# Optimization experiments

Measured on AMD Instinct MI355X. Metric: run time of the kernel, lower is better.

Reference implementation:

```python
import jax, jax.numpy as jnp
import numpy as np
from jax import lax

CAP = 15.0
EPS = 1e-6

def _rmsnorm(x, w):
    xf = x.astype(jnp.float32)
    var = jnp.mean(xf * xf, axis=-1, keepdims=True)
    return w * (xf * lax.rsqrt(var + EPS)).astype(x.dtype)

def _softcap_sigmoid(x):
    return jax.nn.sigmoid(CAP * jnp.tanh(x / CAP))

def setup_inputs() -> dict:
    key = jax.random.key(0)
    ks = jax.random.split(key, 4)
    B, S, D, P = 8, 2048, 1024, 1365
    x = jax.random.normal(ks[0], (B, S, D), dtype=jnp.float32)
    h0 = jnp.zeros((B, P), dtype=jnp.float32)
    ln_weight = jnp.ones((D,), dtype=jnp.float32)
    gate_w = jax.random.normal(ks[1], (3 * P, D), dtype=jnp.float32) * 0.02
    cell_w = jax.random.normal(ks[2], (P, D), dtype=jnp.float32) * 0.02
    out_w = jax.random.normal(ks[3], (D, P), dtype=jnp.float32) * 0.02
    return {"x": x, "h0": h0, "ln_weight": ln_weight, "gate_w": gate_w,
            "cell_w": cell_w, "out_w": out_w}

def reference(x, h0, ln_weight, gate_w, cell_w, out_w):
    B, S, D = x.shape
    P = cell_w.shape[0]
    residual = x
    xn = _rmsnorm(x, ln_weight)
    # gates: [B,S,3P] -> [B,S,3,P]
    gates = jnp.einsum('bsd,gd->bsg', xn, gate_w).reshape(B, S, 3, P)
    g = _softcap_sigmoid(gates)
    i_gate, f_gate, o_gate = g[:, :, 0], g[:, :, 1], g[:, :, 2]
    c_input = jnp.einsum('bsd,pd->bsp', xn, cell_w)
    # sequential sLSTM recurrence over time via scan; xs are time-major [S,B,P]
    xs = (jnp.swapaxes(c_input, 0, 1), jnp.swapaxes(i_gate, 0, 1),
          jnp.swapaxes(f_gate, 0, 1), jnp.swapaxes(o_gate, 0, 1))
    def step(h, ts):
        c_t, i_t, f_t, o_t = ts
        h = f_t * h + i_t * jnp.tanh(c_t)
        return h, o_t * jnp.tanh(h)
    h_final, ys = lax.scan(step, h0, xs)
    output = jnp.swapaxes(ys, 0, 1)  # [B,S,P]
    out = residual + jnp.einsum('bsp,dp->bsd', output, out_w)
    return (out, h_final)
```

## Files before the change

### kernel.cpp

```cpp
#include <hip/hip_runtime.h>
#include <hip/hip_bf16.h>
#include <cstdint>

#define B_   8
#define S_   2048
#define D_   1024
#define P_   1365
#define M_   (B_*S_)
#define KP   1408
#define NGCP (4*KP)
#define CHUNK 32
#define CMAX (S_/CHUNK)

typedef __attribute__((ext_vector_type(8))) short bf16x8;
typedef __attribute__((ext_vector_type(4))) float f32x4;

__device__ __forceinline__ float fast_rcp(float x) {
  return __builtin_amdgcn_rcpf(x);
}
__device__ __forceinline__ float fast_tanh(float x) {
  float e = __expf(2.0f * x);
  return 1.0f - 2.0f * fast_rcp(e + 1.0f);
}
__device__ __forceinline__ float softcap_sig(float x) {
  float u = x * (1.0f / 15.0f);
  float z = -x + x * u * u * (1.0f / 3.0f);
  return fast_rcp(1.0f + __expf(z));
}
__device__ __forceinline__ float bf2f(unsigned short u) {
  union { float f; unsigned int i; } x; x.i = ((unsigned)u) << 16; return x.f;
}
__device__ __forceinline__ unsigned short f2bf(float f) {
  __hip_bfloat16 h = __float2bfloat16(f);
  return *reinterpret_cast<unsigned short*>(&h);
}
__device__ __forceinline__ void gload_lds16(const void* g, void* l) {
  __builtin_amdgcn_global_load_lds(
      (const __attribute__((address_space(1))) uint32_t*)g,
      (__attribute__((address_space(3))) uint32_t*)l,
      16, 0, 0);
}

__global__ void k_prep_wgc(const float* __restrict__ gate_w,
                           const float* __restrict__ cell_w,
                           __hip_bfloat16* __restrict__ wgc) {
  int gid = blockIdx.x * blockDim.x + threadIdx.x;
  int idx = gid * 4;
  int r = idx >> 10, c = idx & 1023;
  int g = r / KP;
  int rr = r - g * KP;
  float4 v;
  if (rr < P_) {
    if (g < 3) v = *(const float4*)(gate_w + (size_t)(g * P_ + rr) * D_ + c);
    else       v = *(const float4*)(cell_w + (size_t)rr * D_ + c);
  } else v = make_float4(0.f, 0.f, 0.f, 0.f);
  __hip_bfloat16* dst = wgc + idx;
  dst[0] = __float2bfloat16(v.x); dst[1] = __float2bfloat16(v.y);
  dst[2] = __float2bfloat16(v.z); dst[3] = __float2bfloat16(v.w);
}

__global__ void k_prep_wout(const float* __restrict__ out_w,
                            __hip_bfloat16* __restrict__ wout) {
  int gid = blockIdx.x * blockDim.x + threadIdx.x;
  int idx = gid * 4;
  int d = idx / KP, p = idx - d * KP;
  __hip_bfloat16* dst = wout + idx;
  #pragma unroll
  for (int j = 0; j < 4; ++j) {
    int pp = p + j;
    float v = (pp < P_) ? out_w[(size_t)d * P_ + pp] : 0.f;
    dst[j] = __float2bfloat16(v);
  }
}

__global__ __launch_bounds__(256) void k_rmsnorm(const float* __restrict__ x,
                                                 const float* __restrict__ w,
                                                 __hip_bfloat16* __restrict__ xn) {
  __shared__ float red[4];
  int m = blockIdx.x;
  int tid = threadIdx.x;
  float4 v = ((const float4*)(x + (size_t)m * D_))[tid];
  float ss = v.x * v.x + v.y * v.y + v.z * v.z + v.w * v.w;
  #pragma unroll
  for (int off = 32; off > 0; off >>= 1) ss += __shfl_down(ss, off);
  if ((tid & 63) == 0) red[tid >> 6] = ss;
  __syncthreads();
  float tot = red[0] + red[1] + red[2] + red[3];
  float scale = rsqrtf(tot * (1.0f / (float)D_) + 1e-6f);
  float4 wv = ((const float4*)w)[tid];
  __hip_bfloat16* o = xn + (size_t)m * D_ + tid * 4;
  o[0] = __float2bfloat16(v.x * scale * wv.x);
  o[1] = __float2bfloat16(v.y * scale * wv.y);
  o[2] = __float2bfloat16(v.z * scale * wv.z);
  o[3] = __float2bfloat16(v.w * scale * wv.w);
}

template<int LDK, int KT, bool GATES>
__global__ __launch_bounds__(512) void k_gemm256(
    const __hip_bfloat16* __restrict__ A,
    const __hip_bfloat16* __restrict__ Bw,
    __hip_bfloat16* __restrict__ pi, __hip_bfloat16* __restrict__ pf,
    __hip_bfloat16* __restrict__ po, __hip_bfloat16* __restrict__ ptc,
    const float* __restrict__ xres, float* __restrict__ out,
    int s0, int sc_shift, int NBY) {
  __shared__ __align__(16) __hip_bfloat16 lA[2][256 * 64];
  __shared__ __align__(16) __hip_bfloat16 lB[2][256 * 64];
  const int tid = threadIdx.x;
  const int lane = tid & 63;
  const int wid = tid >> 6;
  const int wm = wid >> 2, wn = wid & 3;
  const int lr = lane & 15, lg = lane >> 4;
  const int bx = blockIdx.x / NBY;
  const int by = blockIdx.x % NBY;
  const int rl0 = by * 256;
  const int col0 = bx * 256;
  const int scm = (1 << sc_shift) - 1;

  auto grow_of = [&](int rl) -> size_t {
    int bb = rl >> sc_shift;
    return (size_t)bb * S_ + s0 + (rl & scm);
  };

  auto stage = [&](int buf, int kt) {
    const int k0 = kt * 64;
    #pragma unroll
    for (int ld = 0; ld < 4; ++ld) {
      int off = (ld * 512 + tid) * 8;
      int r = off >> 6, c = off & 63;
      int csrc = c ^ ((r & 7) << 3);
      size_t ar = GATES ? grow_of(rl0 + r) : (size_t)(rl0 + r);
      gload_lds16(A + ar * LDK + k0 + csrc, &lA[buf][off]);
    }
    #pragma unroll
    for (int ld = 0; ld < 4; ++ld) {
      int off = (ld * 512 + tid) * 8;
      int r = off >> 6, c = off & 63;
      int csrc = c ^ ((r & 7) << 3);
      gload_lds16(Bw + (size_t)(col0 + r) * LDK + k0 + csrc, &lB[buf][off]);
    }
  };

  const f32x4 zero = {0.f, 0.f, 0.f, 0.f};
  f32x4 acc[8][4];
  #pragma unroll
  for (int i = 0; i < 8; ++i)
    #pragma unroll
    for (int j = 0; j < 4; ++j) acc[i][j] = zero;

  stage(0, 0);
  __syncthreads();
  for (int kt = 0; kt < KT; ++kt) {
    const int cur = kt & 1;
    if (kt + 1 < KT) stage(cur ^ 1, kt + 1);
    #pragma unroll
    for (int ks = 0; ks < 2; ++ks) {
      bf16x8 af[8], bfr[4];
      #pragma unroll
      for (int mi = 0; mi < 8; ++mi) {
        int R = wm * 128 + mi * 16 + lr;
        int ec = (ks * 32 + lg * 8) ^ ((R & 7) << 3);
        af[mi] = *(const bf16x8*)&lA[cur][R * 64 + ec];
      }
      #pragma unroll
      for (int ni = 0; ni < 4; ++ni) {
        int R = wn * 64 + ni * 16 + lr;
        int ec = (ks * 32 + lg * 8) ^ ((R & 7) << 3);
        bfr[ni] = *(const bf16x8*)&lB[cur][R * 64 + ec];
      }
      #pragma unroll
      for (int mi = 0; mi < 8; ++mi)
        #pragma unroll
        for (int ni = 0; ni < 4; ++ni)
          acc[mi][ni] = __builtin_amdgcn_mfma_f32_16x16x32_bf16(af[mi], bfr[ni], acc[mi][ni], 0, 0, 0);
    }
    __syncthreads();
  }

  if (GATES) {
    #pragma unroll
    for (int ni = 0; ni < 4; ++ni) {
      int gn = col0 + wn * 64 + ni * 16 + lr;
      int g = gn / KP;
      int p = gn - g * KP;
      __hip_bfloat16* plane = (g == 0) ? pi : (g == 1) ? pf : (g == 2) ? po : ptc;
      const bool istanh = (g == 3);
      #pragma unroll
      for (int mi = 0; mi < 8; ++mi) {
        #pragma unroll
        for (int j = 0; j < 4; ++j) {
          int rl = rl0 + wm * 128 + mi * 16 + lg * 4 + j;
          float v = acc[mi][ni][j];
          float r = istanh ? fast_tanh(v) : softcap_sig(v);
          plane[(size_t)rl * KP + p] = __float2bfloat16(r);
        }
      }
    }
  } else {
    #pragma unroll
    for (int ni = 0; ni < 4; ++ni) {
      int gn = col0 + wn * 64 + ni * 16 + lr;
      #pragma unroll
      for (int mi = 0; mi < 8; ++mi) {
        #pragma unroll
        for (int j = 0; j < 4; ++j) {
          int rl = rl0 + wm * 128 + mi * 16 + lg * 4 + j;
          size_t o = grow_of(rl) * D_ + gn;
          out[o] = xres[o] + acc[mi][ni][j];
        }
      }
    }
  }
}

__global__ __launch_bounds__(256) void k_scan_p1(
    const __hip_bfloat16* __restrict__ pi, const __hip_bfloat16* __restrict__ pf,
    const __hip_bfloat16* __restrict__ ptc,
    float* __restrict__ Abuf, float* __restrict__ Bbuf, int C) {
  int t = blockIdx.x * blockDim.x + threadIdx.x;
  int p4 = t % (KP / 4);
  int rest = t / (KP / 4);
  int b = rest & 7;
  int c = rest >> 3;
  int p = p4 * 4;
  size_t base = ((size_t)b * C * CHUNK + (size_t)c * CHUNK) * KP + p;
  float4 Aa = make_float4(1.f, 1.f, 1.f, 1.f);
  float4 Bc = make_float4(0.f, 0.f, 0.f, 0.f);
  #pragma unroll 8
  for (int sl = 0; sl < CHUNK; ++sl) {
    size_t idx = base + (size_t)sl * KP;
    ushort4 vf = *reinterpret_cast<const ushort4*>(pf + idx);
    ushort4 vi = *reinterpret_cast<const ushort4*>(pi + idx);
    ushort4 vt = *reinterpret_cast<const ushort4*>(ptc + idx);
    float f0 = bf2f(vf.x), f1 = bf2f(vf.y), f2 = bf2f(vf.z), f3 = bf2f(vf.w);
    Aa.x *= f0; Aa.y *= f1; Aa.z *= f2; Aa.w *= f3;
    Bc.x = f0 * Bc.x + bf2f(vi.x) * bf2f(vt.x);
    Bc.y = f1 * Bc.y + bf2f(vi.y) * bf2f(vt.y);
    Bc.z = f2 * Bc.z + bf2f(vi.z) * bf2f(vt.z);
    Bc.w = f3 * Bc.w + bf2f(vi.w) * bf2f(vt.w);
  }
  size_t o = ((size_t)c * B_ + b) * KP + p;
  *reinterpret_cast<float4*>(Abuf + o) = Aa;
  *reinterpret_cast<float4*>(Bbuf + o) = Bc;
}

__global__ __launch_bounds__(256) void k_scan_p2(
    const float* __restrict__ Abuf, const float* __restrict__ Bbuf,
    const float* __restrict__ h_in, float* __restrict__ carry,
    float* __restrict__ h_out, int C) {
  int t = blockIdx.x * blockDim.x + threadIdx.x;
  int b = t / KP;
  int p = t - b * KP;
  float h = (p < P_) ? h_in[(size_t)b * P_ + p] : 0.f;
  #pragma unroll 8
  for (int c = 0; c < C; ++c) {
    size_t o = ((size_t)c * B_ + b) * KP + p;
    carry[o] = h;
    h = Abuf[o] * h + Bbuf[o];
  }
  if (p < P_) h_out[(size_t)b * P_ + p] = h;
}

__global__ __launch_bounds__(256) void k_scan_p3(
    const __hip_bfloat16* __restrict__ pi, const __hip_bfloat16* __restrict__ pf,
    const __hip_bfloat16* __restrict__ po, __hip_bfloat16* __restrict__ ptc,
    const float* __restrict__ carry, int C) {
  int t = blockIdx.x * blockDim.x + threadIdx.x;
  int p4 = t % (KP / 4);
  int rest = t / (KP / 4);
  int b = rest & 7;
  int c = rest >> 3;
  int p = p4 * 4;
  float4 h4 = *reinterpret_cast<const float4*>(carry + ((size_t)c * B_ + b) * KP + p);
  size_t base = ((size_t)b * C * CHUNK + (size_t)c * CHUNK) * KP + p;
  #pragma unroll 4
  for (int sl = 0; sl < CHUNK; ++sl) {
    size_t idx = base + (size_t)sl * KP;
    ushort4 vf = *reinterpret_cast<const ushort4*>(pf + idx);
    ushort4 vi = *reinterpret_cast<const ushort4*>(pi + idx);
    ushort4 vo = *reinterpret_cast<const ushort4*>(po + idx);
    ushort4 vt = *reinterpret_cast<const ushort4*>(ptc + idx);
    h4.x = bf2f(vf.x) * h4.x + bf2f(vi.x) * bf2f(vt.x);
    h4.y = bf2f(vf.y) * h4.y + bf2f(vi.y) * bf2f(vt.y);
    h4.z = bf2f(vf.z) * h4.z + bf2f(vi.z) * bf2f(vt.z);
    h4.w = bf2f(vf.w) * h4.w + bf2f(vi.w) * bf2f(vt.w);
    ushort4 y;
    y.x = f2bf(bf2f(vo.x) * fast_tanh(h4.x));
    y.y = f2bf(bf2f(vo.y) * fast_tanh(h4.y));
    y.z = f2bf(bf2f(vo.z) * fast_tanh(h4.z));
    y.w = f2bf(bf2f(vo.w) * fast_tanh(h4.w));
    *reinterpret_cast<ushort4*>(ptc + idx) = y;
  }
}

extern "C" void kernel_launch(void* const* d_in, const int* in_sizes, int n_in,
                              void* d_out, int out_size, void* d_ws, size_t ws_size,
                              hipStream_t stream) {
  const float* x      = (const float*)d_in[0];
  const float* h0     = (const float*)d_in[1];
  const float* lnw    = (const float*)d_in[2];
  const float* gate_w = (const float*)d_in[3];
  const float* cell_w = (const float*)d_in[4];
  const float* out_w  = (const float*)d_in[5];
  float* out  = (float*)d_out;
  float* hfin = out + (size_t)M_ * D_;

  size_t off = 0;
  char* ws = (char*)d_ws;
  __hip_bfloat16* xn   = (__hip_bfloat16*)(ws + off); off += (size_t)M_ * D_ * 2;
  __hip_bfloat16* wgc  = (__hip_bfloat16*)(ws + off); off += (size_t)NGCP * D_ * 2;
  __hip_bfloat16* wout = (__hip_bfloat16*)(ws + off); off += (size_t)D_ * KP * 2;
  float* hbuf          = (float*)(ws + off);          off += (size_t)B_ * P_ * 4;
  float* Abuf          = (float*)(ws + off);          off += (size_t)CMAX * B_ * KP * 4;
  float* Bbuf          = (float*)(ws + off);          off += (size_t)CMAX * B_ * KP * 4;
  float* carry         = (float*)(ws + off);          off += (size_t)CMAX * B_ * KP * 4;
  off = (off + 255) & ~(size_t)255;

  int nchunks = 1;
  while (nchunks < 16) {
    size_t planes = 4ull * B_ * (S_ / nchunks) * KP * 2;
    if (off + planes <= ws_size) break;
    nchunks <<= 1;
  }
  const int Sc = S_ / nchunks;
  const int C = Sc / CHUNK;
  int sc_shift = 0;
  while ((1 << sc_shift) < Sc) ++sc_shift;
  __hip_bfloat16* pi  = (__hip_bfloat16*)(ws + off); off += (size_t)B_ * Sc * KP * 2;
  __hip_bfloat16* pf  = (__hip_bfloat16*)(ws + off); off += (size_t)B_ * Sc * KP * 2;
  __hip_bfloat16* po  = (__hip_bfloat16*)(ws + off); off += (size_t)B_ * Sc * KP * 2;
  __hip_bfloat16* ptc = (__hip_bfloat16*)(ws + off); off += (size_t)B_ * Sc * KP * 2;

  k_prep_wgc<<<dim3(NGCP * D_ / 1024), dim3(256), 0, stream>>>(gate_w, cell_w, wgc);
  k_prep_wout<<<dim3(D_ * KP / 1024), dim3(256), 0, stream>>>(out_w, wout);
  k_rmsnorm<<<dim3(M_), dim3(256), 0, stream>>>(x, lnw, xn);

  for (int c = 0; c < nchunks; ++c) {
    int s0 = c * Sc;
    const int NBY = B_ * Sc / 256;
    k_gemm256<D_, D_/64, true><<<dim3((NGCP / 256) * NBY), dim3(512), 0, stream>>>(
        xn, wgc, pi, pf, po, ptc, nullptr, nullptr, s0, sc_shift, NBY);
    int np1 = B_ * C * (KP / 4);
    k_scan_p1<<<dim3(np1 / 256), dim3(256), 0, stream>>>(pi, pf, ptc, Abuf, Bbuf, C);
    k_scan_p2<<<dim3(B_ * KP / 256), dim3(256), 0, stream>>>(
        Abuf, Bbuf, (c == 0) ? h0 : hbuf, carry,
        (c == nchunks - 1) ? hfin : hbuf, C);
    k_scan_p3<<<dim3(np1 / 256), dim3(256), 0, stream>>>(pi, pf, po, ptc, carry, C);
    k_gemm256<KP, KP/64, false><<<dim3((D_ / 256) * NBY), dim3(512), 0, stream>>>(
        ptc, wout, nullptr, nullptr, nullptr, nullptr, x, out, s0, sc_shift, NBY);
  }
}
```

Baseline: 479.5 us.

## Restructure GEMM main loop into 8-phase interleaved half-tile staging with raw barriers

Rewrites the bf16 MFMA GEMM main loop as a two-tile unrolled schedule that splits each k-tile's A and B global-to-LDS loads into halves. The half loads are interleaved between quarter-blocks of MFMAs, separated by raw s_barrier calls with manual vmcnt waits and s_setprio raised around the compute. It also adds a minimum of 2 blocks per CU to the launch bounds. The aim is to hide global load latency behind the matrix ops and to keep the MFMA units busy. In exchange, the synchronisation becomes fragile: it relies on hand-counted vmcnt values and assumes KT is even. Register pressure under the 2-block bound may cause spills.

New measurement: 479.5 us. About the same (+0.0%).

```diff
diff --git a/kernel.cpp b/kernel.cpp
--- a/kernel.cpp
+++ b/kernel.cpp
@@ -40,6 +40,9 @@
       (__attribute__((address_space(3))) uint32_t*)l,
       16, 0, 0);
 }
+
+#define BAR do { asm volatile("" ::: "memory"); __builtin_amdgcn_s_barrier(); \
+                 asm volatile("" ::: "memory"); } while (0)
 
 __global__ void k_prep_wgc(const float* __restrict__ gate_w,
                            const float* __restrict__ cell_w,
@@ -96,7 +99,7 @@
 }
 
 template<int LDK, int KT, bool GATES>
-__global__ __launch_bounds__(512) void k_gemm256(
+__global__ __launch_bounds__(512, 2) void k_gemm256(
     const __hip_bfloat16* __restrict__ A,
     const __hip_bfloat16* __restrict__ Bw,
     __hip_bfloat16* __restrict__ pi, __hip_bfloat16* __restrict__ pf,
@@ -121,23 +124,33 @@
     return (size_t)bb * S_ + s0 + (rl & scm);
   };
 
-  auto stage = [&](int buf, int kt) {
-    const int k0 = kt * 64;
-    #pragma unroll
-    for (int ld = 0; ld < 4; ++ld) {
-      int off = (ld * 512 + tid) * 8;
-      int r = off >> 6, c = off & 63;
+  auto stage_half = [&](int t, int arr, int h) {
+    const int buf = t & 1;
+    const int k0 = t * 64;
+    #pragma unroll
+    for (int l = 0; l < 2; ++l) {
+      int s = l * 512 + tid;
+      int r = h * 128 + (s >> 3);
+      int c = (s & 7) * 8;
       int csrc = c ^ ((r & 7) << 3);
-      size_t ar = GATES ? grow_of(rl0 + r) : (size_t)(rl0 + r);
-      gload_lds16(A + ar * LDK + k0 + csrc, &lA[buf][off]);
+      if (arr == 0) {
+        size_t ar = GATES ? grow_of(rl0 + r) : (size_t)(rl0 + r);
+        gload_lds16(A + ar * LDK + k0 + csrc, &lA[buf][r * 64 + c]);
+      } else {
+        gload_lds16(Bw + (size_t)(col0 + r) * LDK + k0 + csrc, &lB[buf][r * 64 + c]);
+      }
     }
-    #pragma unroll
-    for (int ld = 0; ld < 4; ++ld) {
-      int off = (ld * 512 + tid) * 8;
-      int r = off >> 6, c = off & 63;
-      int csrc = c ^ ((r & 7) << 3);
-      gload_lds16(Bw + (size_t)(col0 + r) * LDK + k0 + csrc, &lB[buf][off]);
-    }
+  };
+
+  auto rdA = [&](int buf, int mi, int ks) -> bf16x8 {
+    int R = wm * 128 + mi * 16 + lr;
+    int ec = (ks * 32 + lg * 8) ^ ((R & 7) << 3);
+    return *(const bf16x8*)&lA[buf][R * 64 + ec];
+  };
+  auto rdB = [&](int buf, int ni, int ks) -> bf16x8 {
+    int R = wn * 64 + ni * 16 + lr;
+    int ec = (ks * 32 + lg * 8) ^ ((R & 7) << 3);
+    return *(const bf16x8*)&lB[buf][R * 64 + ec];
   };
 
   const f32x4 zero = {0.f, 0.f, 0.f, 0.f};
@@ -147,33 +160,135 @@
     #pragma unroll
     for (int j = 0; j < 4; ++j) acc[i][j] = zero;
 
-  stage(0, 0);
-  __syncthreads();
-  for (int kt = 0; kt < KT; ++kt) {
-    const int cur = kt & 1;
-    if (kt + 1 < KT) stage(cur ^ 1, kt + 1);
-    #pragma unroll
-    for (int ks = 0; ks < 2; ++ks) {
-      bf16x8 af[8], bfr[4];
-      #pragma unroll
-      for (int mi = 0; mi < 8; ++mi) {
-        int R = wm * 128 + mi * 16 + lr;
-        int ec = (ks * 32 + lg * 8) ^ ((R & 7) << 3);
-        af[mi] = *(const bf16x8*)&lA[cur][R * 64 + ec];
-      }
-      #pragma unroll
-      for (int ni = 0; ni < 4; ++ni) {
-        int R = wn * 64 + ni * 16 + lr;
-        int ec = (ks * 32 + lg * 8) ^ ((R & 7) << 3);
-        bfr[ni] = *(const bf16x8*)&lB[cur][R * 64 + ec];
-      }
-      #pragma unroll
-      for (int mi = 0; mi < 8; ++mi)
-        #pragma unroll
-        for (int ni = 0; ni < 4; ++ni)
-          acc[mi][ni] = __builtin_amdgcn_mfma_f32_16x16x32_bf16(af[mi], bfr[ni], acc[mi][ni], 0, 0, 0);
-    }
-    __syncthreads();
+  stage_half(0, 1, 0); stage_half(0, 1, 1);
+  stage_half(0, 0, 0); stage_half(0, 0, 1);
+  stage_half(1, 1, 0); stage_half(1, 1, 1);
+  asm volatile("s_waitcnt vmcnt(4)" ::: "memory");
+  BAR;
+
+  const int ITERS = KT / 2;
+  for (int i = 0; i < ITERS; ++i) {
+    const bool lastIt = (i == ITERS - 1);
+    const int o = 2 * i + 1, t2 = 2 * i + 2, t3 = 2 * i + 3;
+    bf16x8 af[4][2], bfr[4][2];
+
+    #pragma unroll
+    for (int mi = 0; mi < 4; ++mi) { af[mi][0] = rdA(0, mi, 0); af[mi][1] = rdA(0, mi, 1); }
+    #pragma unroll
+    for (int ni = 0; ni < 2; ++ni) { bfr[ni][0] = rdB(0, ni, 0); bfr[ni][1] = rdB(0, ni, 1); }
+    stage_half(o, 0, 0);
+    BAR;
+    __builtin_amdgcn_s_setprio(1);
+    #pragma unroll
+    for (int mi = 0; mi < 4; ++mi)
+      #pragma unroll
+      for (int ni = 0; ni < 2; ++ni)
+        #pragma unroll
+        for (int ks = 0; ks < 2; ++ks)
+          acc[mi][ni] = __builtin_amdgcn_mfma_f32_16x16x32_bf16(af[mi][ks], bfr[ni][ks], acc[mi][ni], 0, 0, 0);
+    __builtin_amdgcn_s_setprio(0);
+    BAR;
+    #pragma unroll
+    for (int ni = 2; ni < 4; ++ni) { bfr[ni][0] = rdB(0, ni, 0); bfr[ni][1] = rdB(0, ni, 1); }
+    stage_half(o, 0, 1);
+    BAR;
+    __builtin_amdgcn_s_setprio(1);
+    #pragma unroll
+    for (int mi = 0; mi < 4; ++mi)
+      #pragma unroll
+      for (int ni = 2; ni < 4; ++ni)
+        #pragma unroll
+        for (int ks = 0; ks < 2; ++ks)
+          acc[mi][ni] = __builtin_amdgcn_mfma_f32_16x16x32_bf16(af[mi][ks], bfr[ni][ks], acc[mi][ni], 0, 0, 0);
+    __builtin_amdgcn_s_setprio(0);
+    BAR;
+    #pragma unroll
+    for (int mi = 0; mi < 4; ++mi) { af[mi][0] = rdA(0, mi + 4, 0); af[mi][1] = rdA(0, mi + 4, 1); }
+    if (t2 < KT) stage_half(t2, 1, 0);
+    BAR;
+    __builtin_amdgcn_s_setprio(1);
+    #pragma unroll
+    for (int mi = 0; mi < 4; ++mi)
+      #pragma unroll
+      for (int ni = 2; ni < 4; ++ni)
+        #pragma unroll
+        for (int ks = 0; ks < 2; ++ks)
+          acc[mi + 4][ni] = __builtin_amdgcn_mfma_f32_16x16x32_bf16(af[mi][ks], bfr[ni][ks], acc[mi + 4][ni], 0, 0, 0);
+    __builtin_amdgcn_s_setprio(0);
+    BAR;
+    if (t2 < KT) stage_half(t2, 1, 1);
+    BAR;
+    __builtin_amdgcn_s_setprio(1);
+    #pragma unroll
+    for (int mi = 0; mi < 4; ++mi)
+      #pragma unroll
+      for (int ni = 0; ni < 2; ++ni)
+        #pragma unroll
+        for (int ks = 0; ks < 2; ++ks)
+          acc[mi + 4][ni] = __builtin_amdgcn_mfma_f32_16x16x32_bf16(af[mi][ks], bfr[ni][ks], acc[mi + 4][ni], 0, 0, 0);
+    __builtin_amdgcn_s_setprio(0);
+    if (lastIt) { asm volatile("s_waitcnt vmcnt(0)" ::: "memory"); }
+    else        { asm volatile("s_waitcnt vmcnt(4)" ::: "memory"); }
+    BAR;
+
+    #pragma unroll
+    for (int mi = 0; mi < 4; ++mi) { af[mi][0] = rdA(1, mi, 0); af[mi][1] = rdA(1, mi, 1); }
+    #pragma unroll
+    for (int ni = 0; ni < 2; ++ni) { bfr[ni][0] = rdB(1, ni, 0); bfr[ni][1] = rdB(1, ni, 1); }
+    if (t2 < KT) stage_half(t2, 0, 0);
+    BAR;
+    __builtin_amdgcn_s_setprio(1);
+    #pragma unroll
+    for (int mi = 0; mi < 4; ++mi)
+      #pragma unroll
+      for (int ni = 0; ni < 2; ++ni)
+        #pragma unroll
+        for (int ks = 0; ks < 2; ++ks)
+          acc[mi][ni] = __builtin_amdgcn_mfma_f32_16x16x32_bf16(af[mi][ks], bfr[ni][ks], acc[mi][ni], 0, 0, 0);
+    __builtin_amdgcn_s_setprio(0);
+    BAR;
+    #pragma unroll
+    for (int ni = 2; ni < 4; ++ni) { bfr[ni][0] = rdB(1, ni, 0); bfr[ni][1] = rdB(1, ni, 1); }
+    if (t2 < KT) stage_half(t2, 0, 1);
+    BAR;
+    __builtin_amdgcn_s_setprio(1);
+    #pragma unroll
+    for (int mi = 0; mi < 4; ++mi)
+      #pragma unroll
+      for (int ni = 2; ni < 4; ++ni)
+        #pragma unroll
+        for (int ks = 0; ks < 2; ++ks)
+          acc[mi][ni] = __builtin_amdgcn_mfma_f32_16x16x32_bf16(af[mi][ks], bfr[ni][ks], acc[mi][ni], 0, 0, 0);
+    __builtin_amdgcn_s_setprio(0);
+    BAR;
+    #pragma unroll
+    for (int mi = 0; mi < 4; ++mi) { af[mi][0] = rdA(1, mi + 4, 0); af[mi][1] = rdA(1, mi + 4, 1); }
+    if (t3 < KT) stage_half(t3, 1, 0);
+    BAR;
+    __builtin_amdgcn_s_setprio(1);
+    #pragma unroll
+    for (int mi = 0; mi < 4; ++mi)
+      #pragma unroll
+      for (int ni = 2; ni < 4; ++ni)
+        #pragma unroll
+        for (int ks = 0; ks < 2; ++ks)
+          acc[mi + 4][ni] = __builtin_amdgcn_mfma_f32_16x16x32_bf16(af[mi][ks], bfr[ni][ks], acc[mi + 4][ni], 0, 0, 0);
+    __builtin_amdgcn_s_setprio(0);
+    BAR;
+    if (t3 < KT) stage_half(t3, 1, 1);
+    BAR;
+    __builtin_amdgcn_s_setprio(1);
+    #pragma unroll
+    for (int mi = 0; mi < 4; ++mi)
+      #pragma unroll
+      for (int ni = 0; ni < 2; ++ni)
+        #pragma unroll
+        for (int ks = 0; ks < 2; ++ks)
+          acc[mi + 4][ni] = __builtin_amdgcn_mfma_f32_16x16x32_bf16(af[mi][ks], bfr[ni][ks], acc[mi + 4][ni], 0, 0, 0);
+    __builtin_amdgcn_s_setprio(0);
+    if (lastIt) { asm volatile("s_waitcnt vmcnt(0)" ::: "memory"); }
+    else        { asm volatile("s_waitcnt vmcnt(4)" ::: "memory"); }
+    BAR;
   }
 
   if (GATES) {
@@ -204,8 +319,8 @@
         #pragma unroll
         for (int j = 0; j < 4; ++j) {
           int rl = rl0 + wm * 128 + mi * 16 + lg * 4 + j;
-          size_t o = grow_of(rl) * D_ + gn;
-          out[o] = xres[o] + acc[mi][ni][j];
+          size_t o2 = grow_of(rl) * D_ + gn;
+          out[o2] = xres[o2] + acc[mi][ni][j];
         }
       }
     }
```

## Stage gate GEMM epilogue through LDS and remap blocks across XCDs

Applied to the files above, without the earlier changes.

The gate GEMM epilogue now writes its activated bf16 tile into shared memory first. It then stores whole rows to the output planes as 16-byte vectors, replacing the old scattered 2-byte stores. The block index is also remapped so consecutive tiles are spread across the 8 XCD groups, aiming for better L2 locality. The cost is an extra LDS round trip and a barrier. The remap also assumes the grid size divides evenly by 8.

After: 443.5 us. 1.08x faster.

```diff
diff --git a/kernel.cpp b/kernel.cpp
--- a/kernel.cpp
+++ b/kernel.cpp
@@ -103,15 +103,20 @@
     __hip_bfloat16* __restrict__ po, __hip_bfloat16* __restrict__ ptc,
     const float* __restrict__ xres, float* __restrict__ out,
     int s0, int sc_shift, int NBY) {
-  __shared__ __align__(16) __hip_bfloat16 lA[2][256 * 64];
-  __shared__ __align__(16) __hip_bfloat16 lB[2][256 * 64];
+  __shared__ __align__(16) char smem[131072];
+  __hip_bfloat16* ldsA = (__hip_bfloat16*)smem;
+  __hip_bfloat16* ldsB = (__hip_bfloat16*)(smem + 65536);
   const int tid = threadIdx.x;
   const int lane = tid & 63;
   const int wid = tid >> 6;
   const int wm = wid >> 2, wn = wid & 3;
   const int lr = lane & 15, lg = lane >> 4;
-  const int bx = blockIdx.x / NBY;
-  const int by = blockIdx.x % NBY;
+
+  const int NX = gridDim.x / NBY;
+  const int cpx = gridDim.x >> 3;
+  const int w2 = (blockIdx.x & 7) * cpx + (blockIdx.x >> 3);
+  const int by = w2 / NX;
+  const int bx = w2 - by * NX;
   const int rl0 = by * 256;
   const int col0 = bx * 256;
   const int scm = (1 << sc_shift) - 1;
@@ -124,19 +129,13 @@
   auto stage = [&](int buf, int kt) {
     const int k0 = kt * 64;
     #pragma unroll
-    for (int ld = 0; ld < 4; ++ld) {
-      int off = (ld * 512 + tid) * 8;
+    for (int it = 0; it < 4; ++it) {
+      int off = (it * 512 + tid) * 8;
       int r = off >> 6, c = off & 63;
       int csrc = c ^ ((r & 7) << 3);
       size_t ar = GATES ? grow_of(rl0 + r) : (size_t)(rl0 + r);
-      gload_lds16(A + ar * LDK + k0 + csrc, &lA[buf][off]);
-    }
-    #pragma unroll
-    for (int ld = 0; ld < 4; ++ld) {
-      int off = (ld * 512 + tid) * 8;
-      int r = off >> 6, c = off & 63;
-      int csrc = c ^ ((r & 7) << 3);
-      gload_lds16(Bw + (size_t)(col0 + r) * LDK + k0 + csrc, &lB[buf][off]);
+      if (it < 2) gload_lds16(A + ar * LDK + k0 + csrc, ldsA + buf * 16384 + off);
+      gload_lds16(Bw + (size_t)(col0 + r) * LDK + k0 + csrc, ldsB + buf * 16384 + off);
     }
   };
 
@@ -147,11 +146,24 @@
     #pragma unroll
     for (int j = 0; j < 4; ++j) acc[i][j] = zero;
 
-  stage(0, 0);
+  auto stage_full = [&](int buf, int kt) {
+    const int k0 = kt * 64;
+    #pragma unroll
+    for (int it = 0; it < 4; ++it) {
+      int off = (it * 512 + tid) * 8;
+      int r = off >> 6, c = off & 63;
+      int csrc = c ^ ((r & 7) << 3);
+      size_t ar = GATES ? grow_of(rl0 + r) : (size_t)(rl0 + r);
+      gload_lds16(A + ar * LDK + k0 + csrc, ldsA + buf * 16384 + off);
+      gload_lds16(Bw + (size_t)(col0 + r) * LDK + k0 + csrc, ldsB + buf * 16384 + off);
+    }
+  };
+
+  stage_full(0, 0);
   __syncthreads();
   for (int kt = 0; kt < KT; ++kt) {
     const int cur = kt & 1;
-    if (kt + 1 < KT) stage(cur ^ 1, kt + 1);
+    if (kt + 1 < KT) stage_full(cur ^ 1, kt + 1);
     #pragma unroll
     for (int ks = 0; ks < 2; ++ks) {
       bf16x8 af[8], bfr[4];
@@ -159,13 +171,13 @@
       for (int mi = 0; mi < 8; ++mi) {
         int R = wm * 128 + mi * 16 + lr;
         int ec = (ks * 32 + lg * 8) ^ ((R & 7) << 3);
-        af[mi] = *(const bf16x8*)&lA[cur][R * 64 + ec];
+        af[mi] = *(const bf16x8*)&ldsA[cur * 16384 + R * 64 + ec];
       }
       #pragma unroll
       for (int ni = 0; ni < 4; ++ni) {
         int R = wn * 64 + ni * 16 + lr;
         int ec = (ks * 32 + lg * 8) ^ ((R & 7) << 3);
-        bfr[ni] = *(const bf16x8*)&lB[cur][R * 64 + ec];
+        bfr[ni] = *(const bf16x8*)&ldsB[cur * 16384 + R * 64 + ec];
       }
       #pragma unroll
       for (int mi = 0; mi < 8; ++mi)
@@ -177,35 +189,47 @@
   }
 
   if (GATES) {
+    __hip_bfloat16* Ct = (__hip_bfloat16*)smem;
+    #pragma unroll
+    for (int ni = 0; ni < 4; ++ni) {
+      int cc = wn * 64 + ni * 16 + lr;
+      int g = (col0 + wn * 64 + ni * 16) / KP;
+      const bool istanh = (g == 3);
+      #pragma unroll
+      for (int mi = 0; mi < 8; ++mi) {
+        #pragma unroll
+        for (int j = 0; j < 4; ++j) {
+          int rr = wm * 128 + mi * 16 + lg * 4 + j;
+          float v = acc[mi][ni][j];
+          Ct[rr * 256 + cc] = __float2bfloat16(istanh ? fast_tanh(v) : softcap_sig(v));
+        }
+      }
+    }
+    __syncthreads();
+    #pragma unroll
+    for (int it = 0; it < 16; ++it) {
+      int idx = it * 512 + tid;
+      int rr = idx >> 5;
+      int ck = idx & 31;
+      int gn8 = col0 + ck * 8;
+      int g = gn8 / KP;
+      int p = gn8 - g * KP;
+      __hip_bfloat16* plane = (g == 0) ? pi : (g == 1) ? pf : (g == 2) ? po : ptc;
+      size_t rl = (size_t)(rl0 + rr);
+      *reinterpret_cast<float4*>(&plane[rl * KP + p]) =
+          *reinterpret_cast<const float4*>(&Ct[rr * 256 + ck * 8]);
+    }
+  } else {
     #pragma unroll
     for (int ni = 0; ni < 4; ++ni) {
       int gn = col0 + wn * 64 + ni * 16 + lr;
-      int g = gn / KP;
-      int p = gn - g * KP;
-      __hip_bfloat16* plane = (g == 0) ? pi : (g == 1) ? pf : (g == 2) ? po : ptc;
-      const bool istanh = (g == 3);
       #pragma unroll
       for (int mi = 0; mi < 8; ++mi) {
         #pragma unroll
         for (int j = 0; j < 4; ++j) {
           int rl = rl0 + wm * 128 + mi * 16 + lg * 4 + j;
-          float v = acc[mi][ni][j];
-          float r = istanh ? fast_tanh(v) : softcap_sig(v);
-          plane[(size_t)rl * KP + p] = __float2bfloat16(r);
-        }
-      }
-    }
-  } else {
-    #pragma unroll
-    for (int ni = 0; ni < 4; ++ni) {
-      int gn = col0 + wn * 64 + ni * 16 + lr;
-      #pragma unroll
-      for (int mi = 0; mi < 8; ++mi) {
-        #pragma unroll
-        for (int j = 0; j < 4; ++j) {
-          int rl = rl0 + wm * 128 + mi * 16 + lg * 4 + j;
-          size_t o = grow_of(rl) * D_ + gn;
-          out[o] = xres[o] + acc[mi][ni][j];
+          size_t o2 = grow_of(rl) * D_ + gn;
+          out[o2] = xres[o2] + acc[mi][ni][j];
         }
       }
     }
```
